# Optimization experiments

Measured on AMD Instinct MI355X. Metric: run time of the kernel, lower is better.

## Reference

```python
import jax, jax.numpy as jnp
import numpy as np

N = 100000
E = 3200000
IN_C = 512
HID = 64
OP_C = 64
OUT_C = 2


def setup_inputs() -> dict:
    key = jax.random.key(0)
    ks = jax.random.split(key, 12)
    x = jax.random.normal(ks[0], (N, IN_C), dtype=jnp.float32)
    edge_index = jax.random.randint(ks[1], (2, E), 0, N, dtype=jnp.int32)
    edge_attr = jax.random.uniform(ks[2], (E,), dtype=jnp.float32)
    op = jax.random.normal(ks[3], (N, OP_C), dtype=jnp.float32)
    s1 = 1.0 / np.sqrt(IN_C)
    s2 = 1.0 / np.sqrt(HID)
    s3 = 1.0 / np.sqrt(IN_C + OP_C)
    W1 = jax.random.uniform(ks[4], (IN_C, HID), jnp.float32, -s1, s1)
    b1 = jnp.zeros((HID,), jnp.float32)
    W2 = jax.random.uniform(ks[5], (HID, HID), jnp.float32, -s2, s2)
    b2 = jnp.zeros((HID,), jnp.float32)
    Wp = jax.random.uniform(ks[6], (HID, IN_C), jnp.float32, -s2, s2)
    bp = jax.random.uniform(ks[7], (IN_C,), jnp.float32, -s2, s2)
    Wfc = jax.random.uniform(ks[8], (IN_C + OP_C, OUT_C), jnp.float32, -s3, s3)
    bfc = jax.random.uniform(ks[9], (OUT_C,), jnp.float32, -s3, s3)
    return {"x": x, "edge_index": edge_index, "edge_attr": edge_attr, "op": op,
            "W1": W1, "b1": b1, "W2": W2, "b2": b2,
            "Wp": Wp, "bp": bp, "Wfc": Wfc, "bfc": bfc}


def _gcn_conv(x, W, b, row, col, w):
    # PyG GCNConv: add self-loops (weight 1), symmetric normalization,
    # messages flow source(row) -> target(col).
    h = x @ W  # [N, out]
    loop = jnp.arange(N, dtype=row.dtype)
    row_f = jnp.concatenate([row, loop])
    col_f = jnp.concatenate([col, loop])
    w_f = jnp.concatenate([w, jnp.ones((N,), w.dtype)])
    deg = jax.ops.segment_sum(w_f, col_f, num_segments=N)
    dinv = jnp.where(deg > 0, jax.lax.rsqrt(jnp.maximum(deg, 1e-30)), 0.0)
    norm = dinv[row_f] * w_f * dinv[col_f]  # [E+N]
    msg = norm[:, None] * h[row_f]          # gather + weight
    out = jax.ops.segment_sum(msg, col_f, num_segments=N)  # scatter-add
    return out + b


def reference(x, edge_index, edge_attr, op, W1, b1, W2, b2, Wp, bp, Wfc, bfc):
    row, col = edge_index[0], edge_index[1]
    w = 1.0 / (edge_attr + 1.0)
    h = jax.nn.relu(_gcn_conv(x, W1, b1, row, col, w))   # dropout = identity (eval)
    h = jax.nn.relu(_gcn_conv(h, W2, b2, row, col, w))
    emb = h @ Wp + bp
    z = jnp.concatenate([emb, op], axis=1)
    return z @ Wfc + bfc
```

## Files before the change

### kernel.cpp

```cpp
#include <hip/hip_runtime.h>
#include <hip/hip_bf16.h>

#define IN_C 512
#define HID 64
#define OP_C 64
#define OUT_C 2

#define NPB 256
#define NPB_SHIFT 8
#define MAXB 512
#define BINB 1024
#define EPT 8
#define EPB (BINB*EPT)
#define WFIX 16777216.0f

using bf16x8 = __attribute__((ext_vector_type(8))) short;
using f32x4  = __attribute__((ext_vector_type(4))) float;

static __device__ __forceinline__ unsigned short f2bf(float f) {
    unsigned int u = __float_as_uint(f);
    u = (u + 0x7FFFu + ((u >> 16) & 1u)) >> 16;
    return (unsigned short)u;
}
static __device__ __forceinline__ float bf2f(unsigned short s) {
    return __uint_as_float(((unsigned int)s) << 16);
}

static __device__ __forceinline__ unsigned long long pack_e(int src, int lc, float w) {
    return ((unsigned long long)lc << 49) | ((unsigned long long)(unsigned)src << 32)
         | (unsigned long long)__float_as_uint(w);
}

static __device__ __forceinline__ void wprep_one(const float* __restrict__ W,
                                                 unsigned short* __restrict__ wfrag, int idx) {
    int e  = idx & 7;
    int l  = (idx >> 3) & 63;
    int nf = (idx >> 9) & 3;
    int kt = idx >> 11;
    int k  = kt * 32 + (l >> 4) * 8 + e;
    int c  = nf * 16 + (l & 15);
    wfrag[idx] = f2bf(W[k * 64 + c]);
}

__global__ __launch_bounds__(256) void setup_k(const float* __restrict__ Wp,
                                               const float* __restrict__ bp,
                                               const float* __restrict__ Wfc,
                                               const float* __restrict__ bfc,
                                               float* M, float* cvec,
                                               const float* __restrict__ W1,
                                               unsigned short* __restrict__ wfrag1,
                                               const float* __restrict__ W2,
                                               unsigned short* __restrict__ wfrag2,
                                               int* gcnt, int B) {
    int b = blockIdx.x, t = threadIdx.x;
    if (b == 0) {
        if (t < 128) {
            int k = t >> 1, j = t & 1;
            float s = 0.f;
            for (int f = 0; f < IN_C; ++f) s += Wp[k * IN_C + f] * Wfc[f * 2 + j];
            M[t] = s;
        } else if (t < 130) {
            int j = t - 128;
            float s = bfc[j];
            for (int f = 0; f < IN_C; ++f) s += bp[f] * Wfc[f * 2 + j];
            cvec[j] = s;
        }
    } else if (b <= 128) {
        wprep_one(W1, wfrag1, (b - 1) * 256 + t);
    } else if (b <= 144) {
        wprep_one(W2, wfrag2, (b - 129) * 256 + t);
    } else {
        int i = (b - 145) * 256 + t;
        if (i < B) gcnt[i] = 0;
    }
}

__global__ __launch_bounds__(BINB) void p1a_k(const int* __restrict__ col,
                                              int* __restrict__ gcnt,
                                              int* __restrict__ blk_off,
                                              int E, int B) {
    __shared__ int hist[MAXB];
    int tid = threadIdx.x;
    long e0 = (long)blockIdx.x * EPB;
    for (int i = tid; i < B; i += BINB) hist[i] = 0;
    __syncthreads();
    #pragma unroll
    for (int j = 0; j < EPT; ++j) {
        long e = e0 + j * BINB + tid;
        if (e < E) atomicAdd(&hist[col[e] >> NPB_SHIFT], 1);
    }
    __syncthreads();
    for (int b = tid; b < B; b += BINB) {
        int h = hist[b];
        if (h > 0) blk_off[(long)blockIdx.x * B + b] = atomicAdd(&gcnt[b], h);
    }
}

__global__ __launch_bounds__(256) void scanB_k(const int* __restrict__ gcnt,
                                               int* __restrict__ bptr, int B, int E) {
    __shared__ int lds[256];
    int t = threadIdx.x;
    int v[4]; int s = 0;
    #pragma unroll
    for (int j = 0; j < 4; ++j) { int i = t * 4 + j; v[j] = (i < B) ? gcnt[i] : 0; s += v[j]; }
    lds[t] = s; __syncthreads();
    int x = s;
    for (int off = 1; off < 256; off <<= 1) {
        int y = (t >= off) ? lds[t - off] : 0;
        __syncthreads();
        x += y; lds[t] = x;
        __syncthreads();
    }
    int p = x - s;
    #pragma unroll
    for (int j = 0; j < 4; ++j) { int i = t * 4 + j; if (i < B) bptr[i] = p; p += v[j]; }
    if (t == 255) bptr[B] = E;
}

__global__ __launch_bounds__(BINB) void p1b_k(const int* __restrict__ row,
                                              const int* __restrict__ col,
                                              const float* __restrict__ attr,
                                              const int* __restrict__ blk_off,
                                              const int* __restrict__ bptr,
                                              unsigned long long* __restrict__ binned,
                                              int E, int B) {
    __shared__ int cur[MAXB];
    int tid = threadIdx.x;
    long e0 = (long)blockIdx.x * EPB;
    for (int i = tid; i < B; i += BINB) cur[i] = 0;
    __syncthreads();
    #pragma unroll
    for (int j = 0; j < EPT; ++j) {
        long e = e0 + j * BINB + tid;
        if (e < E) {
            int c = col[e];
            int b = c >> NPB_SHIFT;
            int r = atomicAdd(&cur[b], 1);
            int pos = bptr[b] + blk_off[(long)blockIdx.x * B + b] + r;
            float w = 1.0f / (attr[e] + 1.0f);
            binned[pos] = pack_e(row[e], c & (NPB - 1), w);
        }
    }
}

__global__ __launch_bounds__(256) void p2_k(const unsigned long long* __restrict__ binned,
                                            const int* __restrict__ bptr,
                                            int2* __restrict__ edges,
                                            int* __restrict__ rowptr,
                                            float* __restrict__ dinv,
                                            int N, int E) {
    __shared__ int cnt[NPB];
    __shared__ unsigned int fxw[NPB];
    __shared__ int excl[NPB];
    __shared__ int cur[NPB];
    __shared__ float dvl[NPB];
    int tid = threadIdx.x;
    int b = blockIdx.x;
    int e0 = bptr[b], e1 = bptr[b + 1];
    int c0 = b << NPB_SHIFT;
    cnt[tid] = 0; fxw[tid] = 0; cur[tid] = 0;
    if (b == 0 && tid == 0) rowptr[N] = E;
    __syncthreads();
    for (int i = e0 + tid; i < e1; i += 256) {
        unsigned long long p = binned[i];
        int lc = (int)(p >> 49);
        float w = __uint_as_float((unsigned int)p);
        atomicAdd(&cnt[lc], 1);
        atomicAdd(&fxw[lc], (unsigned int)(w * WFIX));
    }
    __syncthreads();
    excl[tid] = cnt[tid];
    __syncthreads();
    for (int off = 1; off < NPB; off <<= 1) {
        int v = (tid >= off) ? excl[tid - off] : 0;
        __syncthreads();
        excl[tid] += v;
        __syncthreads();
    }
    {
        int ex = excl[tid] - cnt[tid];
        excl[tid] = ex;
        int c = c0 + tid;
        if (c < N) {
            rowptr[c] = e0 + ex;
            float deg = 1.0f + (float)((double)fxw[tid] * (1.0 / 16777216.0));
            float dv = rsqrtf(deg);
            dinv[c] = dv;
            dvl[tid] = dv;
        }
    }
    __syncthreads();
    for (int i = e0 + tid; i < e1; i += 256) {
        unsigned long long p = binned[i];
        int lc = (int)(p >> 49);
        int src = (int)((p >> 32) & 0x1FFFF);
        float w = __uint_as_float((unsigned int)p);
        int r = atomicAdd(&cur[lc], 1);
        float nrm_p = w * dvl[lc];
        edges[e0 + excl[lc] + r] = make_int2(src, __float_as_int(nrm_p));
    }
}

__global__ __launch_bounds__(512) void gemm1_k(const float* __restrict__ A,
                                               const unsigned short* __restrict__ wfrag,
                                               const float* __restrict__ dinv,
                                               unsigned short* __restrict__ out, int M) {
    __shared__ unsigned short wlds[32768];
    int tid = threadIdx.x;
    {
        const float4* s4 = (const float4*)wfrag;
        float4* d4 = (float4*)wlds;
        #pragma unroll
        for (int i = 0; i < 8; ++i) d4[tid + 512 * i] = s4[tid + 512 * i];
    }
    __syncthreads();
    int wv = tid >> 6, l = tid & 63;
    int lg = l >> 4, lr = l & 15;
    long band = (long)blockIdx.x * 128 + wv * 16;
    long row = band + lr;
    long rowc = row < M ? row : (long)(M - 1);
    const float* xp = A + rowc * IN_C + lg * 8;
    f32x4 acc0 = {0.f,0.f,0.f,0.f}, acc1 = {0.f,0.f,0.f,0.f};
    f32x4 acc2 = {0.f,0.f,0.f,0.f}, acc3 = {0.f,0.f,0.f,0.f};
    #pragma unroll 4
    for (int kt = 0; kt < 16; ++kt) {
        float4 xa = *(const float4*)(xp + kt * 32);
        float4 xb = *(const float4*)(xp + kt * 32 + 4);
        bf16x8 a;
        a[0] = (short)f2bf(xa.x); a[1] = (short)f2bf(xa.y);
        a[2] = (short)f2bf(xa.z); a[3] = (short)f2bf(xa.w);
        a[4] = (short)f2bf(xb.x); a[5] = (short)f2bf(xb.y);
        a[6] = (short)f2bf(xb.z); a[7] = (short)f2bf(xb.w);
        const bf16x8* bp = (const bf16x8*)&wlds[kt * 4 * 64 * 8 + l * 8];
        acc0 = __builtin_amdgcn_mfma_f32_16x16x32_bf16(a, bp[0],   acc0, 0, 0, 0);
        acc1 = __builtin_amdgcn_mfma_f32_16x16x32_bf16(a, bp[64],  acc1, 0, 0, 0);
        acc2 = __builtin_amdgcn_mfma_f32_16x16x32_bf16(a, bp[128], acc2, 0, 0, 0);
        acc3 = __builtin_amdgcn_mfma_f32_16x16x32_bf16(a, bp[192], acc3, 0, 0, 0);
    }
    #pragma unroll
    for (int r = 0; r < 4; ++r) {
        long orow = band + lg * 4 + r;
        if (orow < M) {
            float dv = dinv[orow];
            out[orow * 64 +  0 + lr] = f2bf(acc0[r] * dv);
            out[orow * 64 + 16 + lr] = f2bf(acc1[r] * dv);
            out[orow * 64 + 32 + lr] = f2bf(acc2[r] * dv);
            out[orow * 64 + 48 + lr] = f2bf(acc3[r] * dv);
        }
    }
}

__global__ __launch_bounds__(512) void gemm2_k(const unsigned short* __restrict__ A2,
                                               const unsigned short* __restrict__ wfrag,
                                               const float* __restrict__ dinv,
                                               unsigned short* __restrict__ out, int M) {
    __shared__ unsigned short wlds[4096];
    int tid = threadIdx.x;
    ((float4*)wlds)[tid] = ((const float4*)wfrag)[tid];
    __syncthreads();
    int wv = tid >> 6, l = tid & 63;
    int lg = l >> 4, lr = l & 15;
    long band = (long)blockIdx.x * 128 + wv * 16;
    long row = band + lr;
    long rowc = row < M ? row : (long)(M - 1);
    const unsigned short* ap = A2 + rowc * 64 + lg * 8;
    f32x4 acc0 = {0.f,0.f,0.f,0.f}, acc1 = {0.f,0.f,0.f,0.f};
    f32x4 acc2 = {0.f,0.f,0.f,0.f}, acc3 = {0.f,0.f,0.f,0.f};
    #pragma unroll
    for (int kt = 0; kt < 2; ++kt) {
        bf16x8 a = *(const bf16x8*)(ap + kt * 32);
        const bf16x8* bp = (const bf16x8*)&wlds[kt * 4 * 64 * 8 + l * 8];
        acc0 = __builtin_amdgcn_mfma_f32_16x16x32_bf16(a, bp[0],   acc0, 0, 0, 0);
        acc1 = __builtin_amdgcn_mfma_f32_16x16x32_bf16(a, bp[64],  acc1, 0, 0, 0);
        acc2 = __builtin_amdgcn_mfma_f32_16x16x32_bf16(a, bp[128], acc2, 0, 0, 0);
        acc3 = __builtin_amdgcn_mfma_f32_16x16x32_bf16(a, bp[192], acc3, 0, 0, 0);
    }
    #pragma unroll
    for (int r = 0; r < 4; ++r) {
        long orow = band + lg * 4 + r;
        if (orow < M) {
            float dv = dinv[orow];
            out[orow * 64 +  0 + lr] = f2bf(acc0[r] * dv);
            out[orow * 64 + 16 + lr] = f2bf(acc1[r] * dv);
            out[orow * 64 + 32 + lr] = f2bf(acc2[r] * dv);
            out[orow * 64 + 48 + lr] = f2bf(acc3[r] * dv);
        }
    }
}

__device__ __forceinline__ void agg_core(const unsigned short* __restrict__ h2,
                                         const int* __restrict__ rowptr,
                                         const int2* __restrict__ edges,
                                         const float* __restrict__ dinv,
                                         const float* __restrict__ bias,
                                         int node, int l,
                                         float& acc0, float& acc1) {
    float di = dinv[node];
    ushort2 hv = *(const ushort2*)(h2 + (size_t)node * 64 + 2 * l);
    acc0 = di * bf2f(hv.x);
    acc1 = di * bf2f(hv.y);
    int s = rowptr[node], e = rowptr[node + 1];
    int li = l & 15;
    for (int base = s; base < e; base += 16) {
        int mm = e - base; mm = mm > 16 ? 16 : mm;
        int2 my = edges[base + (li < mm ? li : 0)];
        if (mm == 16) {
            #pragma unroll
            for (int j = 0; j < 16; ++j) {
                int srcj = __shfl(my.x, j, 32);
                float nj = __int_as_float(__shfl(my.y, j, 32));
                ushort2 q = *(const ushort2*)(h2 + (size_t)srcj * 64 + 2 * l);
                acc0 += nj * bf2f(q.x);
                acc1 += nj * bf2f(q.y);
            }
        } else {
            for (int j = 0; j < mm; ++j) {
                int srcj = __shfl(my.x, j, 32);
                float nj = __int_as_float(__shfl(my.y, j, 32));
                ushort2 q = *(const ushort2*)(h2 + (size_t)srcj * 64 + 2 * l);
                acc0 += nj * bf2f(q.x);
                acc1 += nj * bf2f(q.y);
            }
        }
    }
    float2 bb = *(const float2*)(bias + 2 * l);
    acc0 = fmaxf(acc0 + bb.x, 0.0f);
    acc1 = fmaxf(acc1 + bb.y, 0.0f);
}

__global__ __launch_bounds__(256) void agg1_k(const unsigned short* __restrict__ h2,
                                              unsigned short* __restrict__ g2,
                                              const int* __restrict__ rowptr,
                                              const int2* __restrict__ edges,
                                              const float* __restrict__ dinv,
                                              const float* __restrict__ bias, int N) {
    int wid = (blockIdx.x * 256 + threadIdx.x) >> 6;
    int lane = threadIdx.x & 63;
    int node = wid * 2 + (lane >> 5);
    int l = lane & 31;
    if (node >= N) return;
    float acc0, acc1;
    agg_core(h2, rowptr, edges, dinv, bias, node, l, acc0, acc1);
    ushort2 o; o.x = f2bf(acc0); o.y = f2bf(acc1);
    *(ushort2*)(g2 + (size_t)node * 64 + 2 * l) = o;
}

__global__ __launch_bounds__(256) void agg2f_k(const unsigned short* __restrict__ h2,
                                               const int* __restrict__ rowptr,
                                               const int2* __restrict__ edges,
                                               const float* __restrict__ dinv,
                                               const float* __restrict__ bias,
                                               const float* __restrict__ op,
                                               const float* __restrict__ M,
                                               const float* __restrict__ Wfc,
                                               const float* __restrict__ cvec,
                                               float* __restrict__ out, int N) {
    int wid = (blockIdx.x * 256 + threadIdx.x) >> 6;
    int lane = threadIdx.x & 63;
    int node = wid * 2 + (lane >> 5);
    int l = lane & 31;
    if (node >= N) return;
    float acc0, acc1;
    agg_core(h2, rowptr, edges, dinv, bias, node, l, acc0, acc1);
    float2 ov = *(const float2*)(op + (size_t)node * 64 + 2 * l);
    int f0 = 2 * l, f1 = 2 * l + 1;
    float p0 = acc0 * M[f0 * 2 + 0] + acc1 * M[f1 * 2 + 0]
             + ov.x * Wfc[(IN_C + f0) * 2 + 0] + ov.y * Wfc[(IN_C + f1) * 2 + 0];
    float p1 = acc0 * M[f0 * 2 + 1] + acc1 * M[f1 * 2 + 1]
             + ov.x * Wfc[(IN_C + f0) * 2 + 1] + ov.y * Wfc[(IN_C + f1) * 2 + 1];
    #pragma unroll
    for (int off = 16; off > 0; off >>= 1) {
        p0 += __shfl_xor(p0, off);
        p1 += __shfl_xor(p1, off);
    }
    if (l == 0)
        *(float2*)(out + (size_t)node * 2) = make_float2(p0 + cvec[0], p1 + cvec[1]);
}

extern "C" void kernel_launch(void* const* d_in, const int* in_sizes, int n_in,
                              void* d_out, int out_size, void* d_ws, size_t ws_size,
                              hipStream_t stream) {
    const float* x    = (const float*)d_in[0];
    const int*   ei   = (const int*)d_in[1];
    const float* attr = (const float*)d_in[2];
    const float* op   = (const float*)d_in[3];
    const float* W1   = (const float*)d_in[4];
    const float* b1   = (const float*)d_in[5];
    const float* W2   = (const float*)d_in[6];
    const float* b2   = (const float*)d_in[7];
    const float* Wp   = (const float*)d_in[8];
    const float* bp   = (const float*)d_in[9];
    const float* Wfc  = (const float*)d_in[10];
    const float* bfc  = (const float*)d_in[11];

    const int N = in_sizes[0] / IN_C;
    const int E = in_sizes[2];
    const int* row = ei;
    const int* col = ei + E;

    const int B     = (N + NPB - 1) >> NPB_SHIFT;
    const int nblk1 = (E + EPB - 1) / EPB;

    char* base = (char*)d_ws;
    size_t off = 0;
    auto alloc = [&](size_t bytes) -> char* {
        char* p = base + off;
        off = (off + bytes + 255) & ~(size_t)255;
        return p;
    };
    int2*  edges  = (int2*)alloc((size_t)E * 8);
    unsigned short* h2 = (unsigned short*)alloc((size_t)N * HID * 2);
    size_t bin_b  = (size_t)E * 8;
    size_t g_b    = (size_t)N * HID * 2;
    char*  regC   = alloc(bin_b > g_b ? bin_b : g_b);
    unsigned long long* binned = (unsigned long long*)regC;
    unsigned short* g2 = (unsigned short*)regC;
    int*   blkoff = (int*)alloc((size_t)nblk1 * B * 4);
    float* dinv   = (float*)alloc((size_t)N * 4);
    int*   rowptr = (int*)alloc((size_t)(N + 1) * 4);
    int*   gcnt   = (int*)alloc((size_t)MAXB * 4);
    int*   bptr   = (int*)alloc((size_t)(MAXB + 1) * 4);
    unsigned short* wfrag1 = (unsigned short*)alloc((size_t)IN_C * 64 * 2);
    unsigned short* wfrag2 = (unsigned short*)alloc((size_t)HID * 64 * 2);
    float* Mbuf   = (float*)alloc(512);
    float* cvec   = (float*)alloc(64);

    const int gAgg  = (((N + 1) / 2) * 64 + 255) / 256;
    const int gGemm = (N + 127) / 128;
    const int gSetup = 145 + (B + 255) / 256;

    setup_k<<<gSetup, 256, 0, stream>>>(Wp, bp, Wfc, bfc, Mbuf, cvec,
                                        W1, wfrag1, W2, wfrag2, gcnt, B);
    p1a_k<<<nblk1, BINB, 0, stream>>>(col, gcnt, blkoff, E, B);
    scanB_k<<<1, 256, 0, stream>>>(gcnt, bptr, B, E);
    p1b_k<<<nblk1, BINB, 0, stream>>>(row, col, attr, blkoff, bptr, binned, E, B);
    p2_k<<<B, 256, 0, stream>>>(binned, bptr, edges, rowptr, dinv, N, E);

    gemm1_k<<<gGemm, 512, 0, stream>>>(x, wfrag1, dinv, h2, N);
    agg1_k<<<gAgg, 256, 0, stream>>>(h2, g2, rowptr, edges, dinv, b1, N);
    gemm2_k<<<gGemm, 512, 0, stream>>>(g2, wfrag2, dinv, h2, N);
    agg2f_k<<<gAgg, 256, 0, stream>>>(h2, rowptr, edges, dinv, b2, op, Mbuf, Wfc, cvec,
                                      (float*)d_out, N);
}
```

Baseline: 333.1 us.

## Stage binned edges in LDS for coalesced writes; use hardware bf16 conversion

The binning kernel now sorts each block's edges by bin into a shared-memory staging buffer using a local prefix scan. It then writes them out contiguously, finding each element's bin by binary search. This aims to replace scattered 8-byte global writes with runs of coalesced writes per bin. The cost is 64KB of LDS per block, which limits occupancy, plus extra syncs and a scan. Separately, the first-layer GEMM switches its fp32-to-bf16 conversion from manual bit rounding to the compiler's native __bf16 cast, which may map to a hardware conversion instruction on gfx950.

```diff
diff --git a/kernel.cpp b/kernel.cpp
--- a/kernel.cpp
+++ b/kernel.cpp
@@ -21,6 +21,10 @@
     unsigned int u = __float_as_uint(f);
     u = (u + 0x7FFFu + ((u >> 16) & 1u)) >> 16;
     return (unsigned short)u;
+}
+static __device__ __forceinline__ short f2bf_hw(float f) {
+    __bf16 h = (__bf16)f;
+    return __builtin_bit_cast(short, h);
 }
 static __device__ __forceinline__ float bf2f(unsigned short s) {
     return __uint_as_float(((unsigned int)s) << 16);
@@ -124,22 +128,58 @@
                                               const int* __restrict__ bptr,
                                               unsigned long long* __restrict__ binned,
                                               int E, int B) {
-    __shared__ int cur[MAXB];
+    __shared__ int gbase[MAXB];
+    __shared__ int loc[MAXB];
+    __shared__ int scanb[512];
+    __shared__ unsigned long long stage[EPB];
     int tid = threadIdx.x;
-    long e0 = (long)blockIdx.x * EPB;
-    for (int i = tid; i < B; i += BINB) cur[i] = 0;
-    __syncthreads();
+    int blk = blockIdx.x;
+    long e0 = (long)blk * EPB;
+    for (int i = tid; i < B; i += BINB) {
+        gbase[i] = bptr[i] + blk_off[(long)blk * B + i];
+        loc[i] = 0;
+    }
+    __syncthreads();
+    unsigned long long pk[EPT]; int eb[EPT]; int er[EPT];
     #pragma unroll
     for (int j = 0; j < EPT; ++j) {
         long e = e0 + j * BINB + tid;
+        eb[j] = -1;
         if (e < E) {
             int c = col[e];
             int b = c >> NPB_SHIFT;
-            int r = atomicAdd(&cur[b], 1);
-            int pos = bptr[b] + blk_off[(long)blockIdx.x * B + b] + r;
             float w = 1.0f / (attr[e] + 1.0f);
-            binned[pos] = pack_e(row[e], c & (NPB - 1), w);
-        }
+            pk[j] = pack_e(row[e], c & (NPB - 1), w);
+            eb[j] = b;
+            er[j] = atomicAdd(&loc[b], 1);
+        }
+    }
+    __syncthreads();
+    if (tid < 512) scanb[tid] = (tid < B) ? loc[tid] : 0;
+    __syncthreads();
+    for (int off = 1; off < 512; off <<= 1) {
+        int y = 0;
+        if (tid < 512 && tid >= off) y = scanb[tid - off];
+        __syncthreads();
+        if (tid < 512) scanb[tid] += y;
+        __syncthreads();
+    }
+    if (tid < B) loc[tid] = scanb[tid] - loc[tid];
+    __syncthreads();
+    #pragma unroll
+    for (int j = 0; j < EPT; ++j)
+        if (eb[j] >= 0) stage[loc[eb[j]] + er[j]] = pk[j];
+    __syncthreads();
+    long rem = E - e0;
+    int ecnt = rem > EPB ? EPB : (int)rem;
+    for (int i = tid; i < ecnt; i += BINB) {
+        int lo = 0, hi = B - 1;
+        #pragma unroll 1
+        while (lo < hi) {
+            int mid = (lo + hi + 1) >> 1;
+            if (loc[mid] <= i) lo = mid; else hi = mid - 1;
+        }
+        binned[gbase[lo] + (i - loc[lo])] = stage[i];
     }
 }
 
@@ -227,10 +267,10 @@
         float4 xa = *(const float4*)(xp + kt * 32);
         float4 xb = *(const float4*)(xp + kt * 32 + 4);
         bf16x8 a;
-        a[0] = (short)f2bf(xa.x); a[1] = (short)f2bf(xa.y);
-        a[2] = (short)f2bf(xa.z); a[3] = (short)f2bf(xa.w);
-        a[4] = (short)f2bf(xb.x); a[5] = (short)f2bf(xb.y);
-        a[6] = (short)f2bf(xb.z); a[7] = (short)f2bf(xb.w);
+        a[0] = f2bf_hw(xa.x); a[1] = f2bf_hw(xa.y);
+        a[2] = f2bf_hw(xa.z); a[3] = f2bf_hw(xa.w);
+        a[4] = f2bf_hw(xb.x); a[5] = f2bf_hw(xb.y);
+        a[6] = f2bf_hw(xb.z); a[7] = f2bf_hw(xb.w);
         const bf16x8* bp = (const bf16x8*)&wlds[kt * 4 * 64 * 8 + l * 8];
         acc0 = __builtin_amdgcn_mfma_f32_16x16x32_bf16(a, bp[0],   acc0, 0, 0, 0);
         acc1 = __builtin_amdgcn_mfma_f32_16x16x32_bf16(a, bp[64],  acc1, 0, 0, 0);
```

Result: faster. 305.3 us (-8.4%).
